# Performance work log

Hardware: AMD Instinct MI355X
Metric: run time of the kernel (lower is better)

The kernel has to match this reference:

```python
import jax, jax.numpy as jnp
import numpy as np

B, NQ, L, E, K = 64, 1024, 128, 8192, 2
LN_EPS = 1e-5


def setup_inputs() -> dict:
    key = jax.random.key(0)
    ks = jax.random.split(key, 16)
    s1 = 1.0 / np.sqrt(2 * L + 1)
    s2 = 1.0 / np.sqrt(L)
    s3 = 1.0 / np.sqrt(2 * L)
    return {
        "z0": jax.random.normal(ks[0], (B, L), jnp.float32),
        "edge_index": jax.random.randint(ks[1], (2, E), 0, NQ, jnp.int64),
        "edge_attr": jax.random.normal(ks[2], (E,), jnp.float32),
        "n_qubits": NQ,
        # edge MLP params, stacked over K message-passing rounds
        "e_w1": jax.random.normal(ks[3], (K, L, 2 * L + 1), jnp.float32) * s1,
        "e_b1": jnp.zeros((K, L), jnp.float32),
        "e_w2": jax.random.normal(ks[4], (K, L, L), jnp.float32) * s2,
        "e_b2": jnp.zeros((K, L), jnp.float32),
        # node MLP params
        "n_w1": jax.random.normal(ks[5], (K, L, 2 * L), jnp.float32) * s3,
        "n_b1": jnp.zeros((K, L), jnp.float32),
        "ln_g": jnp.ones((K, L), jnp.float32),
        "ln_b": jnp.zeros((K, L), jnp.float32),
        "n_w2": jax.random.normal(ks[6], (K, L, L), jnp.float32) * s2,
        "n_b2": jnp.zeros((K, L), jnp.float32),
    }


def reference(z0, edge_index, edge_attr, n_qubits,
              e_w1, e_b1, e_w2, e_b2,
              n_w1, n_b1, ln_g, ln_b, n_w2, n_b2):
    b, l = z0.shape
    src, tgt = edge_index[0], edge_index[1]
    e_ = src.shape[0]
    # broadcast latent z0 to every node: h [B, N, L]
    h = jnp.broadcast_to(z0[:, None, :], (b, n_qubits, l))
    e = jnp.broadcast_to(edge_attr[None, :, None], (b, e_, 1))  # [B, E, 1]
    k_rounds = e_w1.shape[0]
    for k in range(k_rounds):
        hi = h[:, src, :]  # gather source node feats [B, E, L]
        hj = h[:, tgt, :]  # gather target node feats [B, E, L]
        inp_e = jnp.concatenate([hi, hj, e], axis=-1)  # [B, E, 2L+1]
        m = jax.nn.relu(inp_e @ e_w1[k].T + e_b1[k]) @ e_w2[k].T + e_b2[k]
        # scatter_add messages back to source nodes
        m_agg = jnp.zeros_like(h).at[:, src, :].add(m)
        inp_n = jnp.concatenate([h, m_agg], axis=-1)  # [B, N, 2L]
        x = jax.nn.relu(inp_n @ n_w1[k].T + n_b1[k])
        mu = x.mean(axis=-1, keepdims=True)
        var = ((x - mu) ** 2).mean(axis=-1, keepdims=True)
        x = (x - mu) * jax.lax.rsqrt(var + LN_EPS) * ln_g[k] + ln_b[k]
        # Dropout(p=0.1) is identity in eval mode
        h = x @ n_w2[k].T + n_b2[k] + h  # residual
    return h.mean(axis=1)  # [B, L]
```

## Files before the change

### kernel.cpp

```cpp
#include <hip/hip_runtime.h>

#define B_   64
#define NQ_  1024
#define L_   128
#define E_   8192
#define M_   (B_*NQ_)
#define LDP  136

typedef unsigned short u16;
typedef unsigned int   u32;
typedef __attribute__((ext_vector_type(8))) short short8;
typedef __attribute__((ext_vector_type(4))) float floatx4;

#define WVB() __builtin_amdgcn_wave_barrier()

__device__ __forceinline__ u16 f2bf(float f) {
    union { float f; u32 u; } v; v.f = f;
    return (u16)((v.u + 0x7fffu + ((v.u >> 16) & 1u)) >> 16);
}
__device__ __forceinline__ float bf2f(u16 u) {
    union { u32 u; float f; } v; v.u = ((u32)u) << 16;
    return v.f;
}
__device__ __forceinline__ floatx4 mfma16(short8 a, short8 b, floatx4 c) {
    return __builtin_amdgcn_mfma_f32_16x16x32_bf16(a, b, c, 0, 0, 0);
}
__device__ __forceinline__ short8 gfrag(const u16* base, int r0, int kb, int lane) {
    return *(const short8*)(base + (size_t)(r0 + (lane & 15)) * 128 + kb * 32 + (lane >> 4) * 8);
}
__device__ __forceinline__ short8 sfrag(const u16* t, int r0, int kb, int lane) {
    return *(const short8*)(t + (r0 + (lane & 15)) * LDP + kb * 32 + (lane >> 4) * 8);
}
__device__ __forceinline__ short8 frag_cvt(const float* base, int r0, int ld, int kb, int lane) {
    const float* p = base + (size_t)(r0 + (lane & 15)) * ld + kb * 32 + (lane >> 4) * 8;
    short8 s;
#pragma unroll
    for (int j = 0; j < 8; ++j) s[j] = (short)f2bf(p[j]);
    return s;
}
__device__ __forceinline__ void tile_store(u16* t, const floatx4* acc, int lane) {
    int col = lane & 15, qd = lane >> 4;
#pragma unroll
    for (int nt = 0; nt < 8; ++nt)
#pragma unroll
        for (int r = 0; r < 4; ++r)
            t[(qd * 4 + r) * LDP + nt * 16 + col] = f2bf(acc[nt][r]);
}
__device__ __forceinline__ void tile_flush(const u16* t, u16* g, int lane) {
#pragma unroll
    for (int it = 0; it < 4; ++it) {
        int chunk = it * 64 + lane, row = chunk >> 4, c8 = chunk & 15;
        *(uint4*)(g + (size_t)row * 128 + c8 * 8) = *(const uint4*)(t + row * LDP + c8 * 8);
    }
}
__device__ __forceinline__ void stage_w(u16* wbuf, const u16* g, int tid) {
    const uint4* g4 = (const uint4*)g;
#pragma unroll
    for (int i = 0; i < 8; ++i) {
        int idx = tid + i * 256, row = idx >> 4, c8 = idx & 15;
        *(uint4*)&wbuf[row * LDP + c8 * 8] = g4[idx];
    }
}

__global__ __launch_bounds__(256) void k_setup(const int* __restrict__ ei,
                                               const float* __restrict__ attr,
                                               const float* __restrict__ z0,
                                               const float* __restrict__ e_w1,
                                               const float* __restrict__ e_b1,
                                               const float* __restrict__ e_w2,
                                               const float* __restrict__ e_b2,
                                               const float* __restrict__ n_w1,
                                               const float* __restrict__ n_b1,
                                               const float* __restrict__ n_w2,
                                               const float* __restrict__ n_b2,
                                               int* __restrict__ ofs,
                                               int* __restrict__ tgt_s,
                                               float* __restrict__ a_s,
                                               float* __restrict__ degf,
                                               u16* __restrict__ wb,
                                               float* __restrict__ wl,
                                               float* __restrict__ vb2,
                                               float* __restrict__ rx,
                                               float* __restrict__ rci,
                                               float* __restrict__ rcj,
                                               u16* __restrict__ ci0,
                                               u16* __restrict__ cj0) {
    __shared__ __align__(16) char smem[52608];
    int tid = threadIdx.x, blk = blockIdx.x;
    int lane = tid & 63, w = tid >> 6, col = lane & 15, qd = lane >> 4;

    if (blk == 0) {
        int* cnt  = (int*)smem;
        int* wsum = cnt + 1024;
        int* flag = wsum + 8;
#pragma unroll
        for (int i = 0; i < 4; ++i) cnt[tid + i * 256] = 0;
        if (tid == 0) *flag = 1;
        __syncthreads();
        if (tid < 100 && ei[2 * tid + 1] != 0) atomicAnd(flag, 0);
        __syncthreads();
        int i64 = *flag;
        for (int e = tid; e < E_; e += 256) {
            int s = i64 ? ei[2 * e] : ei[e];
            atomicAdd(&cnt[s], 1);
        }
        __syncthreads();
        int q0 = tid * 4;
        int c0 = cnt[q0], c1 = cnt[q0 + 1], c2 = cnt[q0 + 2], c3 = cnt[q0 + 3];
        int tsum = c0 + c1 + c2 + c3, incl = tsum;
#pragma unroll
        for (int o = 1; o < 64; o <<= 1) {
            int t = __shfl_up(incl, o, 64);
            if (lane >= o) incl += t;
        }
        if (lane == 63) wsum[w] = incl;
        __syncthreads();
        int wo = 0;
        for (int i = 0; i < w; ++i) wo += wsum[i];
        int base = wo + incl - tsum;
        ofs[q0] = base; ofs[q0 + 1] = base + c0;
        ofs[q0 + 2] = base + c0 + c1; ofs[q0 + 3] = base + c0 + c1 + c2;
        degf[q0] = (float)c0; degf[q0 + 1] = (float)c1;
        degf[q0 + 2] = (float)c2; degf[q0 + 3] = (float)c3;
        if (tid == 0) ofs[NQ_] = E_;
        __syncthreads();
        cnt[q0] = base; cnt[q0 + 1] = base + c0;
        cnt[q0 + 2] = base + c0 + c1; cnt[q0 + 3] = base + c0 + c1 + c2;
        __syncthreads();
        for (int e = tid; e < E_; e += 256) {
            int s = i64 ? ei[2 * e]        : ei[e];
            int t = i64 ? ei[2 * (E_ + e)] : ei[E_ + e];
            int p = atomicAdd(&cnt[s], 1);
            tgt_s[p] = t;
            a_s[p]   = attr[e];
        }
    } else if (blk <= 3) {
        const float* src; int ld, off; u16* dst;
        if (blk == 1)      { src = n_w2;         ld = 128; off = 0; dst = wb + 1 * 16384; }
        else if (blk == 2) { src = n_w2 + 16384; ld = 128; off = 0; dst = wb + 6 * 16384; }
        else               { src = n_w1 + 32768; ld = 256; off = 0; dst = wb + 4 * 16384; }
        for (int idx = tid; idx < 16384; idx += 256) {
            int n = idx >> 7, kk = idx & 127;
            dst[idx] = f2bf(src[n * ld + off + kk]);
        }
    } else if (blk <= 7) {
        const float* P; const float* Q; int ldp; u16* D;
        if (blk == 4)      { P = n_w1 + 128;           ldp = 256; Q = e_w2;         D = wb;              }
        else if (blk == 5) { P = n_w1 + 32768 + 128;   ldp = 256; Q = e_w2 + 16384; D = wb + 5 * 16384;  }
        else if (blk == 6) { P = e_w1 + 128 * 257;     ldp = 257; Q = n_w2;         D = wb + 2 * 16384;  }
        else               { P = e_w1 + 128 * 257 + 128; ldp = 257; Q = n_w2;       D = wb + 3 * 16384;  }
        u16* qt = (u16*)smem;
        u16* tl = (u16*)(smem + 34816);
        for (int idx = tid; idx < 16384; idx += 256) {
            int c = idx >> 7, kd = idx & 127;
            qt[kd * LDP + c] = f2bf(Q[idx]);
        }
        __syncthreads();
        for (int t = 0; t < 2; ++t) {
            int r0 = (w * 2 + t) * 16;
            floatx4 acc[8] = {};
#pragma unroll
            for (int kb = 0; kb < 4; ++kb) {
                short8 a = frag_cvt(P, r0, ldp, kb, lane);
#pragma unroll
                for (int nt = 0; nt < 8; ++nt)
                    acc[nt] = mfma16(a, sfrag(qt, nt * 16, kb, lane), acc[nt]);
            }
            u16* slot = tl + w * 16 * LDP;
            tile_store(slot, acc, lane); WVB();
            tile_flush(slot, D + (size_t)r0 * 128, lane); WVB();
        }
    } else if (blk == 8) {
        int r0 = w * 16;
        floatx4 acc[8] = {};
#pragma unroll
        for (int kb = 0; kb < 4; ++kb) {
            short8 a = frag_cvt(z0, r0, 128, kb, lane);
#pragma unroll
            for (int nt = 0; nt < 8; ++nt)
                acc[nt] = mfma16(a, frag_cvt(n_w1, nt * 16, 256, kb, lane), acc[nt]);
        }
#pragma unroll
        for (int nt = 0; nt < 8; ++nt) {
            int cg = nt * 16 + col; float bv = n_b1[cg];
#pragma unroll
            for (int r = 0; r < 4; ++r) rx[(r0 + qd * 4 + r) * 128 + cg] = acc[nt][r] + bv;
        }
    } else if (blk == 9 || blk == 10) {
        int r0 = w * 16;
        const float* Wp = (blk == 9) ? (e_w1 + 128 * 257) : (e_w1 + 128 * 257 + 128);
        float* dst = (blk == 9) ? rci : rcj;
        floatx4 acc[8] = {};
#pragma unroll
        for (int kb = 0; kb < 4; ++kb) {
            short8 a;
            int rr = (r0 + (lane & 15)) * 128, kk = kb * 32 + (lane >> 4) * 8;
#pragma unroll
            for (int j = 0; j < 8; ++j) a[j] = (short)f2bf(z0[rr + kk + j] + n_b2[kk + j]);
#pragma unroll
            for (int nt = 0; nt < 8; ++nt)
                acc[nt] = mfma16(a, frag_cvt(Wp, nt * 16, 257, kb, lane), acc[nt]);
        }
#pragma unroll
        for (int nt = 0; nt < 8; ++nt) {
            int cg = nt * 16 + col;
            float bv = (blk == 9) ? e_b1[128 + cg] : 0.0f;
#pragma unroll
            for (int r = 0; r < 4; ++r) dst[(r0 + qd * 4 + r) * 128 + cg] = acc[nt][r] + bv;
        }
    } else if (blk == 11) {
        u16* tl = (u16*)(smem + 34816);
        int r0 = w * 16;
        floatx4 a1[8] = {}, a2[8] = {};
#pragma unroll
        for (int kb = 0; kb < 4; ++kb) {
            short8 a = frag_cvt(z0, r0, 128, kb, lane);
#pragma unroll
            for (int nt = 0; nt < 8; ++nt) {
                a1[nt] = mfma16(a, frag_cvt(e_w1,       nt * 16, 257, kb, lane), a1[nt]);
                a2[nt] = mfma16(a, frag_cvt(e_w1 + 128, nt * 16, 257, kb, lane), a2[nt]);
            }
        }
#pragma unroll
        for (int nt = 0; nt < 8; ++nt) {
            float bv = e_b1[nt * 16 + col];
#pragma unroll
            for (int r = 0; r < 4; ++r) a1[nt][r] += bv;
        }
        u16* slot = tl + w * 16 * LDP;
        tile_store(slot, a1, lane); WVB();
        tile_flush(slot, ci0 + (size_t)r0 * 128, lane); WVB();
        tile_store(slot, a2, lane); WVB();
        tile_flush(slot, cj0 + (size_t)r0 * 128, lane);
    } else {
        int k = tid >> 7, c = tid & 127;
        float s = 0.0f;
        for (int n = 0; n < 128; ++n)
            s += n_w1[k * 32768 + c * 256 + 128 + n] * e_b2[k * 128 + n];
        vb2[tid] = s;
        wl[tid]  = e_w1[k * 128 * 257 + c * 257 + 256];
    }
}

__global__ __launch_bounds__(256) void k_edge(const u16* __restrict__ ci,
                                              const u16* __restrict__ cj,
                                              int ci_bs, int ci_qs,
                                              int cj_bs, int cj_ts,
                                              const int* __restrict__ ofs,
                                              const int* __restrict__ tgt_s,
                                              const float* __restrict__ a_s,
                                              const float* __restrict__ wl,
                                              u16* __restrict__ S) {
    int tid = threadIdx.x, lane = tid & 63, w = tid >> 6;
    int gw = blockIdx.x * 4 + w;
    int q = gw & (NQ_ - 1), b0 = (gw >> 10) * 4;
    const u32* cjp0 = (const u32*)cj + (size_t)(b0 + 0) * cj_bs;
    const u32* cjp1 = (const u32*)cj + (size_t)(b0 + 1) * cj_bs;
    const u32* cjp2 = (const u32*)cj + (size_t)(b0 + 2) * cj_bs;
    const u32* cjp3 = (const u32*)cj + (size_t)(b0 + 3) * cj_bs;
    float cix[4], ciy[4];
#pragma unroll
    for (int i = 0; i < 4; ++i) {
        u32 cv = ((const u32*)ci)[(size_t)(b0 + i) * ci_bs + (size_t)q * ci_qs + lane];
        cix[i] = bf2f((u16)(cv & 0xffff)); ciy[i] = bf2f((u16)(cv >> 16));
    }
    float2 wl2 = ((const float2*)wl)[lane];
    int st = ofs[q], en = ofs[q + 1];
    float ax[4] = {0, 0, 0, 0}, ay[4] = {0, 0, 0, 0};
    for (int idx = st; idx < en; ++idx) {
        int t = tgt_s[idx];
        float a = a_s[idx];
        size_t ro = (size_t)t * cj_ts + lane;
        u32 j0 = cjp0[ro], j1 = cjp1[ro], j2 = cjp2[ro], j3 = cjp3[ro];
        float wx = a * wl2.x, wy = a * wl2.y;
        ax[0] += fmaxf(cix[0] + bf2f((u16)(j0 & 0xffff)) + wx, 0.f);
        ay[0] += fmaxf(ciy[0] + bf2f((u16)(j0 >> 16))    + wy, 0.f);
        ax[1] += fmaxf(cix[1] + bf2f((u16)(j1 & 0xffff)) + wx, 0.f);
        ay[1] += fmaxf(ciy[1] + bf2f((u16)(j1 >> 16))    + wy, 0.f);
        ax[2] += fmaxf(cix[2] + bf2f((u16)(j2 & 0xffff)) + wx, 0.f);
        ay[2] += fmaxf(ciy[2] + bf2f((u16)(j2 >> 16))    + wy, 0.f);
        ax[3] += fmaxf(cix[3] + bf2f((u16)(j3 & 0xffff)) + wx, 0.f);
        ay[3] += fmaxf(ciy[3] + bf2f((u16)(j3 >> 16))    + wy, 0.f);
    }
    u32* Sp = (u32*)S;
#pragma unroll
    for (int i = 0; i < 4; ++i)
        Sp[((size_t)(b0 + i) * NQ_ + q) * 64 + lane] =
            (u32)f2bf(ax[i]) | ((u32)f2bf(ay[i]) << 16);
}

__global__ __launch_bounds__(256, 2) void k_node0(const u16* __restrict__ S,
                                                  const u16* __restrict__ wb,
                                                  const float* __restrict__ rx,
                                                  const float* __restrict__ vb2,
                                                  const float* __restrict__ degf,
                                                  const float* __restrict__ z0,
                                                  const float* __restrict__ n_b2,
                                                  const float* __restrict__ rci,
                                                  const float* __restrict__ rcj,
                                                  const float* __restrict__ g,
                                                  const float* __restrict__ bb,
                                                  u16* __restrict__ hbf,
                                                  u16* __restrict__ ci1,
                                                  u16* __restrict__ cj1,
                                                  float* __restrict__ out) {
    __shared__ u16 wbuf[128 * LDP];
    __shared__ u16 xt[8][16 * LDP];
    __shared__ float rsum[4][128];
    int tid = threadIdx.x, lane = tid & 63, w = tid >> 6;
    int col = lane & 15, qd = lane >> 4;
    int rowbase = blockIdx.x * 128 + w * 32;
    int b = blockIdx.x >> 3;

    stage_w(wbuf, wb, tid);
    __syncthreads();
    floatx4 xa[2][8] = {};
#pragma unroll
    for (int kb = 0; kb < 4; ++kb) {
        short8 Bv[8];
#pragma unroll
        for (int nt = 0; nt < 8; ++nt) Bv[nt] = sfrag(wbuf, nt * 16, kb, lane);
#pragma unroll
        for (int t = 0; t < 2; ++t) {
            short8 a = gfrag(S, rowbase + t * 16, kb, lane);
#pragma unroll
            for (int nt = 0; nt < 8; ++nt) xa[t][nt] = mfma16(a, Bv[nt], xa[t][nt]);
        }
    }
#pragma unroll
    for (int t = 0; t < 2; ++t) {
#pragma unroll
        for (int nt = 0; nt < 8; ++nt) {
            int cg = nt * 16 + col;
            float base = rx[b * 128 + cg], vb = vb2[cg];
#pragma unroll
            for (int r = 0; r < 4; ++r) {
                int row = rowbase + t * 16 + qd * 4 + r;
                xa[t][nt][r] = fmaxf(xa[t][nt][r] + base + degf[row & (NQ_ - 1)] * vb, 0.f);
            }
        }
#pragma unroll
        for (int r = 0; r < 4; ++r) {
            float s = 0.f, s2 = 0.f;
#pragma unroll
            for (int nt = 0; nt < 8; ++nt) { float v = xa[t][nt][r]; s += v; s2 += v * v; }
#pragma unroll
            for (int o = 1; o < 16; o <<= 1) { s += __shfl_xor(s, o, 64); s2 += __shfl_xor(s2, o, 64); }
            float mu = s * (1.f / 128.f), var = s2 * (1.f / 128.f) - mu * mu;
            float rs = rsqrtf(var + 1e-5f);
#pragma unroll
            for (int nt = 0; nt < 8; ++nt) {
                int cg = nt * 16 + col;
                xa[t][nt][r] = (xa[t][nt][r] - mu) * rs * g[cg] + bb[cg];
            }
        }
        tile_store(&xt[w * 2 + t][0], xa[t], lane);
    }
    __syncthreads();

    stage_w(wbuf, wb + 1 * 16384, tid);
    __syncthreads();
    floatx4 ha[2][8] = {};
#pragma unroll
    for (int kb = 0; kb < 4; ++kb) {
        short8 Bv[8];
#pragma unroll
        for (int nt = 0; nt < 8; ++nt) Bv[nt] = sfrag(wbuf, nt * 16, kb, lane);
#pragma unroll
        for (int t = 0; t < 2; ++t) {
            short8 a = sfrag(&xt[w * 2 + t][0], 0, kb, lane);
#pragma unroll
            for (int nt = 0; nt < 8; ++nt) ha[t][nt] = mfma16(a, Bv[nt], ha[t][nt]);
        }
    }
    float s8[8] = {0, 0, 0, 0, 0, 0, 0, 0};
#pragma unroll
    for (int t = 0; t < 2; ++t)
#pragma unroll
        for (int nt = 0; nt < 8; ++nt) {
            int cg = nt * 16 + col;
            float hp = z0[b * 128 + cg] + n_b2[cg];
#pragma unroll
            for (int r = 0; r < 4; ++r) {
                float hv = ha[t][nt][r] + hp;
                ha[t][nt][r] = hv;
                s8[nt] += hv;
            }
        }
#pragma unroll
    for (int nt = 0; nt < 8; ++nt) {
        s8[nt] += __shfl_xor(s8[nt], 16, 64);
        s8[nt] += __shfl_xor(s8[nt], 32, 64);
    }
    if (lane < 16) {
#pragma unroll
        for (int nt = 0; nt < 8; ++nt) rsum[w][nt * 16 + lane] = s8[nt];
    }
    __syncthreads();
    if (tid < 128) {
        float v = rsum[0][tid] + rsum[1][tid] + rsum[2][tid] + rsum[3][tid];
        atomicAdd(out + b * 128 + tid, v * (1.f / 1024.f));
    }
#pragma unroll
    for (int t = 0; t < 2; ++t) tile_store(wbuf + (w * 2 + t) * 16 * LDP, ha[t], lane);
    WVB();
#pragma unroll
    for (int t = 0; t < 2; ++t)
        tile_flush(wbuf + (w * 2 + t) * 16 * LDP, hbf + (size_t)(rowbase + t * 16) * 128, lane);
    __syncthreads();

    stage_w(wbuf, wb + 2 * 16384, tid);
    __syncthreads();
    floatx4 ca[2][8] = {};
#pragma unroll
    for (int kb = 0; kb < 4; ++kb) {
        short8 Bv[8];
#pragma unroll
        for (int nt = 0; nt < 8; ++nt) Bv[nt] = sfrag(wbuf, nt * 16, kb, lane);
#pragma unroll
        for (int t = 0; t < 2; ++t) {
            short8 a = sfrag(&xt[w * 2 + t][0], 0, kb, lane);
#pragma unroll
            for (int nt = 0; nt < 8; ++nt) ca[t][nt] = mfma16(a, Bv[nt], ca[t][nt]);
        }
    }
#pragma unroll
    for (int t = 0; t < 2; ++t)
#pragma unroll
        for (int nt = 0; nt < 8; ++nt) {
            float rc = rci[b * 128 + nt * 16 + col];
#pragma unroll
            for (int r = 0; r < 4; ++r) ca[t][nt][r] += rc;
        }
    __syncthreads();
#pragma unroll
    for (int t = 0; t < 2; ++t) tile_store(wbuf + (w * 2 + t) * 16 * LDP, ca[t], lane);
    WVB();
#pragma unroll
    for (int t = 0; t < 2; ++t)
        tile_flush(wbuf + (w * 2 + t) * 16 * LDP, ci1 + (size_t)(rowbase + t * 16) * 128, lane);
    __syncthreads();

    stage_w(wbuf, wb + 3 * 16384, tid);
    __syncthreads();
    floatx4 da[2][8] = {};
#pragma unroll
    for (int kb = 0; kb < 4; ++kb) {
        short8 Bv[8];
#pragma unroll
        for (int nt = 0; nt < 8; ++nt) Bv[nt] = sfrag(wbuf, nt * 16, kb, lane);
#pragma unroll
        for (int t = 0; t < 2; ++t) {
            short8 a = sfrag(&xt[w * 2 + t][0], 0, kb, lane);
#pragma unroll
            for (int nt = 0; nt < 8; ++nt) da[t][nt] = mfma16(a, Bv[nt], da[t][nt]);
        }
    }
#pragma unroll
    for (int t = 0; t < 2; ++t)
#pragma unroll
        for (int nt = 0; nt < 8; ++nt) {
            float rc = rcj[b * 128 + nt * 16 + col];
#pragma unroll
            for (int r = 0; r < 4; ++r) da[t][nt][r] += rc;
        }
    __syncthreads();
#pragma unroll
    for (int t = 0; t < 2; ++t) tile_store(wbuf + (w * 2 + t) * 16 * LDP, da[t], lane);
    WVB();
#pragma unroll
    for (int t = 0; t < 2; ++t)
        tile_flush(wbuf + (w * 2 + t) * 16 * LDP, cj1 + (size_t)(rowbase + t * 16) * 128, lane);
}

__global__ __launch_bounds__(256, 2) void k_node1(const u16* __restrict__ S,
                                                  const u16* __restrict__ hbf,
                                                  const u16* __restrict__ wb,
                                                  const float* __restrict__ vb2,
                                                  const float* __restrict__ degf,
                                                  const float* __restrict__ n_b1,
                                                  const float* __restrict__ g,
                                                  const float* __restrict__ bb,
                                                  const float* __restrict__ n_b2,
                                                  float* __restrict__ out) {
    __shared__ u16 wbuf[128 * LDP];
    __shared__ u16 xt[8][16 * LDP];
    __shared__ float rsum[4][128];
    int tid = threadIdx.x, lane = tid & 63, w = tid >> 6;
    int col = lane & 15, qd = lane >> 4;
    int rowbase = blockIdx.x * 128 + w * 32;
    int b = blockIdx.x >> 3;

    stage_w(wbuf, wb + 4 * 16384, tid);
    __syncthreads();
    floatx4 xa[2][8] = {};
#pragma unroll
    for (int kb = 0; kb < 4; ++kb) {
        short8 Bv[8];
#pragma unroll
        for (int nt = 0; nt < 8; ++nt) Bv[nt] = sfrag(wbuf, nt * 16, kb, lane);
#pragma unroll
        for (int t = 0; t < 2; ++t) {
            short8 a = gfrag(hbf, rowbase + t * 16, kb, lane);
#pragma unroll
            for (int nt = 0; nt < 8; ++nt) xa[t][nt] = mfma16(a, Bv[nt], xa[t][nt]);
        }
    }
    __syncthreads();
    stage_w(wbuf, wb + 5 * 16384, tid);
    __syncthreads();
#pragma unroll
    for (int kb = 0; kb < 4; ++kb) {
        short8 Bv[8];
#pragma unroll
        for (int nt = 0; nt < 8; ++nt) Bv[nt] = sfrag(wbuf, nt * 16, kb, lane);
#pragma unroll
        for (int t = 0; t < 2; ++t) {
            short8 a = gfrag(S, rowbase + t * 16, kb, lane);
#pragma unroll
            for (int nt = 0; nt < 8; ++nt) xa[t][nt] = mfma16(a, Bv[nt], xa[t][nt]);
        }
    }
#pragma unroll
    for (int t = 0; t < 2; ++t) {
#pragma unroll
        for (int nt = 0; nt < 8; ++nt) {
            int cg = nt * 16 + col;
            float base = n_b1[cg], vb = vb2[cg];
#pragma unroll
            for (int r = 0; r < 4; ++r) {
                int row = rowbase + t * 16 + qd * 4 + r;
                xa[t][nt][r] = fmaxf(xa[t][nt][r] + base + degf[row & (NQ_ - 1)] * vb, 0.f);
            }
        }
#pragma unroll
        for (int r = 0; r < 4; ++r) {
            float s = 0.f, s2 = 0.f;
#pragma unroll
            for (int nt = 0; nt < 8; ++nt) { float v = xa[t][nt][r]; s += v; s2 += v * v; }
#pragma unroll
            for (int o = 1; o < 16; o <<= 1) { s += __shfl_xor(s, o, 64); s2 += __shfl_xor(s2, o, 64); }
            float mu = s * (1.f / 128.f), var = s2 * (1.f / 128.f) - mu * mu;
            float rs = rsqrtf(var + 1e-5f);
#pragma unroll
            for (int nt = 0; nt < 8; ++nt) {
                int cg = nt * 16 + col;
                xa[t][nt][r] = (xa[t][nt][r] - mu) * rs * g[cg] + bb[cg];
            }
        }
        tile_store(&xt[w * 2 + t][0], xa[t], lane);
    }
    __syncthreads();

    stage_w(wbuf, wb + 6 * 16384, tid);
    __syncthreads();
    floatx4 ma[2][8] = {};
#pragma unroll
    for (int kb = 0; kb < 4; ++kb) {
        short8 Bv[8];
#pragma unroll
        for (int nt = 0; nt < 8; ++nt) Bv[nt] = sfrag(wbuf, nt * 16, kb, lane);
#pragma unroll
        for (int t = 0; t < 2; ++t) {
            short8 a = sfrag(&xt[w * 2 + t][0], 0, kb, lane);
#pragma unroll
            for (int nt = 0; nt < 8; ++nt) ma[t][nt] = mfma16(a, Bv[nt], ma[t][nt]);
        }
    }
    float s8[8] = {0, 0, 0, 0, 0, 0, 0, 0};
#pragma unroll
    for (int t = 0; t < 2; ++t)
#pragma unroll
        for (int nt = 0; nt < 8; ++nt)
#pragma unroll
            for (int r = 0; r < 4; ++r) s8[nt] += ma[t][nt][r];
#pragma unroll
    for (int nt = 0; nt < 8; ++nt) {
        s8[nt] += __shfl_xor(s8[nt], 16, 64);
        s8[nt] += __shfl_xor(s8[nt], 32, 64);
    }
    if (lane < 16) {
#pragma unroll
        for (int nt = 0; nt < 8; ++nt) rsum[w][nt * 16 + lane] = s8[nt];
    }
    __syncthreads();
    if (tid < 128) {
        float v = rsum[0][tid] + rsum[1][tid] + rsum[2][tid] + rsum[3][tid];
        atomicAdd(out + b * 128 + tid, v * (1.f / 1024.f) + n_b2[tid] * 0.125f);
    }
}

extern "C" void kernel_launch(void* const* d_in, const int* in_sizes, int n_in,
                              void* d_out, int out_size, void* d_ws, size_t ws_size,
                              hipStream_t stream) {
    const float* z0    = (const float*)d_in[0];
    const int*   ei    = (const int*)d_in[1];
    const float* attr  = (const float*)d_in[2];
    const float* e_w1  = (const float*)d_in[4];
    const float* e_b1  = (const float*)d_in[5];
    const float* e_w2  = (const float*)d_in[6];
    const float* e_b2  = (const float*)d_in[7];
    const float* n_w1  = (const float*)d_in[8];
    const float* n_b1  = (const float*)d_in[9];
    const float* ln_g  = (const float*)d_in[10];
    const float* ln_b  = (const float*)d_in[11];
    const float* n_w2  = (const float*)d_in[12];
    const float* n_b2  = (const float*)d_in[13];
    float* out = (float*)d_out;

    const size_t H = (size_t)M_ * L_;
    float* f    = (float*)d_ws;
    float* degf = f;
    float* a_s  = degf + 1024;
    float* wl   = a_s + 8192;
    float* vb2  = wl + 256;
    float* rx   = vb2 + 256;
    float* rci  = rx + 8192;
    float* rcj  = rci + 8192;
    int*   ofs   = (int*)(rcj + 8192);
    int*   tgt_s = ofs + 1056;
    u16*   wb    = (u16*)(tgt_s + 8192);
    u16*   ci0   = wb + 7 * 16384;
    u16*   cj0   = ci0 + 8192;
    u16*   S     = cj0 + 8192;
    u16*   hbf   = S + H;
    u16*   ci1   = hbf + H;
    u16*   cj1   = ci1 + H;

    hipMemsetAsync(out, 0, 8192 * sizeof(float), stream);

    k_setup<<<13, 256, 0, stream>>>(ei, attr, z0, e_w1, e_b1, e_w2, e_b2,
                                    n_w1, n_b1, n_w2, n_b2,
                                    ofs, tgt_s, a_s, degf, wb, wl, vb2,
                                    rx, rci, rcj, ci0, cj0);

    k_edge<<<4096, 256, 0, stream>>>(ci0, cj0, 64, 0, 64, 0,
                                     ofs, tgt_s, a_s, wl, S);
    k_node0<<<512, 256, 0, stream>>>(S, wb, rx, vb2, degf, z0, n_b2,
                                     rci, rcj, ln_g, ln_b,
                                     hbf, ci1, cj1, out);
    k_edge<<<4096, 256, 0, stream>>>(ci1, cj1, NQ_ * 64, 64, NQ_ * 64, 64,
                                     ofs, tgt_s, a_s, wl + 128, S);
    k_node1<<<512, 256, 0, stream>>>(S, hbf, wb, vb2 + 128, degf,
                                     n_b1 + 128, ln_g + 128, ln_b + 128,
                                     n_b2 + 128, out);
}
```

Before: 197.1 us.

## Fold round-0 node output into next-round projections and specialize first edge pass

Round 0's node output is no longer materialized as h. k_node0 projects the layer-normed activations directly through the folded round-1 weights (h-part of n_w1, ci, cj) and accumulates their per-batch mean into mx0. The final mean is then reconstructed algebraically from mx0 through n_w2 in k_node1. The first edge pass uses a template specialization that exploits the constant per-batch node features, so it skips the target gather by merging the ci and cj contributions into one tensor. Each edge warp now handles 8 batches instead of 4, halving the grid. This moves work between stages, and using an extra bf16 intermediate risks small precision changes.

Result: faster. 190.9 us (-3.2%).

```diff
diff --git a/kernel.cpp b/kernel.cpp
--- a/kernel.cpp
+++ b/kernel.cpp
@@ -83,8 +83,9 @@
                                                float* __restrict__ rx,
                                                float* __restrict__ rci,
                                                float* __restrict__ rcj,
-                                               u16* __restrict__ ci0,
-                                               u16* __restrict__ cj0) {
+                                               float* __restrict__ rh,
+                                               float* __restrict__ mx0,
+                                               u16* __restrict__ c0t) {
     __shared__ __align__(16) char smem[52608];
     int tid = threadIdx.x, blk = blockIdx.x;
     int lane = tid & 63, w = tid >> 6, col = lane & 15, qd = lane >> 4;
@@ -130,25 +131,23 @@
         for (int e = tid; e < E_; e += 256) {
             int s = i64 ? ei[2 * e]        : ei[e];
             int t = i64 ? ei[2 * (E_ + e)] : ei[E_ + e];
-            int p = atomicAdd(&cnt[s], 1);
-            tgt_s[p] = t;
-            a_s[p]   = attr[e];
-        }
-    } else if (blk <= 3) {
-        const float* src; int ld, off; u16* dst;
-        if (blk == 1)      { src = n_w2;         ld = 128; off = 0; dst = wb + 1 * 16384; }
-        else if (blk == 2) { src = n_w2 + 16384; ld = 128; off = 0; dst = wb + 6 * 16384; }
-        else               { src = n_w1 + 32768; ld = 256; off = 0; dst = wb + 4 * 16384; }
-        for (int idx = tid; idx < 16384; idx += 256) {
-            int n = idx >> 7, kk = idx & 127;
-            dst[idx] = f2bf(src[n * ld + off + kk]);
-        }
+            int pos = atomicAdd(&cnt[s], 1);
+            tgt_s[pos] = t;
+            a_s[pos]   = attr[e];
+        }
+    } else if (blk <= 2) {
+        const float* src = (blk == 1) ? n_w2 : (n_w2 + 16384);
+        u16* dst = wb + ((blk == 1) ? 1 : 6) * 16384;
+        for (int idx = tid; idx < 16384; idx += 256) dst[idx] = f2bf(src[idx]);
     } else if (blk <= 7) {
         const float* P; const float* Q; int ldp; u16* D;
-        if (blk == 4)      { P = n_w1 + 128;           ldp = 256; Q = e_w2;         D = wb;              }
-        else if (blk == 5) { P = n_w1 + 32768 + 128;   ldp = 256; Q = e_w2 + 16384; D = wb + 5 * 16384;  }
-        else if (blk == 6) { P = e_w1 + 128 * 257;     ldp = 257; Q = n_w2;         D = wb + 2 * 16384;  }
-        else               { P = e_w1 + 128 * 257 + 128; ldp = 257; Q = n_w2;       D = wb + 3 * 16384;  }
+        switch (blk) {
+            case 3: P = n_w1 + 128;             ldp = 256; Q = e_w2;         D = wb;             break;
+            case 4: P = n_w1 + 32768 + 128;     ldp = 256; Q = e_w2 + 16384; D = wb + 5 * 16384; break;
+            case 5: P = e_w1 + 128 * 257;       ldp = 257; Q = n_w2;         D = wb + 2 * 16384; break;
+            case 6: P = e_w1 + 128 * 257 + 128; ldp = 257; Q = n_w2;         D = wb + 3 * 16384; break;
+            default:P = n_w1 + 32768;           ldp = 256; Q = n_w2;         D = wb + 4 * 16384; break;
+        }
         u16* qt = (u16*)smem;
         u16* tl = (u16*)(smem + 34816);
         for (int idx = tid; idx < 16384; idx += 256) {
@@ -186,10 +185,12 @@
 #pragma unroll
             for (int r = 0; r < 4; ++r) rx[(r0 + qd * 4 + r) * 128 + cg] = acc[nt][r] + bv;
         }
-    } else if (blk == 9 || blk == 10) {
+    } else if (blk <= 11) {
         int r0 = w * 16;
-        const float* Wp = (blk == 9) ? (e_w1 + 128 * 257) : (e_w1 + 128 * 257 + 128);
-        float* dst = (blk == 9) ? rci : rcj;
+        const float* Wp; int ld; const float* bias; float* dst;
+        if (blk == 9)       { Wp = e_w1 + 128 * 257;       ld = 257; bias = e_b1 + 128; dst = rci; }
+        else if (blk == 10) { Wp = e_w1 + 128 * 257 + 128; ld = 257; bias = nullptr;    dst = rcj; }
+        else                { Wp = n_w1 + 32768;           ld = 256; bias = n_b1 + 128; dst = rh;  }
         floatx4 acc[8] = {};
 #pragma unroll
         for (int kb = 0; kb < 4; ++kb) {
@@ -199,26 +200,26 @@
             for (int j = 0; j < 8; ++j) a[j] = (short)f2bf(z0[rr + kk + j] + n_b2[kk + j]);
 #pragma unroll
             for (int nt = 0; nt < 8; ++nt)
-                acc[nt] = mfma16(a, frag_cvt(Wp, nt * 16, 257, kb, lane), acc[nt]);
+                acc[nt] = mfma16(a, frag_cvt(Wp, nt * 16, ld, kb, lane), acc[nt]);
         }
 #pragma unroll
         for (int nt = 0; nt < 8; ++nt) {
             int cg = nt * 16 + col;
-            float bv = (blk == 9) ? e_b1[128 + cg] : 0.0f;
+            float bv = bias ? bias[cg] : 0.0f;
 #pragma unroll
             for (int r = 0; r < 4; ++r) dst[(r0 + qd * 4 + r) * 128 + cg] = acc[nt][r] + bv;
         }
-    } else if (blk == 11) {
+    } else if (blk == 12) {
         u16* tl = (u16*)(smem + 34816);
         int r0 = w * 16;
-        floatx4 a1[8] = {}, a2[8] = {};
+        floatx4 a1[8] = {};
 #pragma unroll
         for (int kb = 0; kb < 4; ++kb) {
             short8 a = frag_cvt(z0, r0, 128, kb, lane);
 #pragma unroll
             for (int nt = 0; nt < 8; ++nt) {
                 a1[nt] = mfma16(a, frag_cvt(e_w1,       nt * 16, 257, kb, lane), a1[nt]);
-                a2[nt] = mfma16(a, frag_cvt(e_w1 + 128, nt * 16, 257, kb, lane), a2[nt]);
+                a1[nt] = mfma16(a, frag_cvt(e_w1 + 128, nt * 16, 257, kb, lane), a1[nt]);
             }
         }
 #pragma unroll
@@ -229,9 +230,7 @@
         }
         u16* slot = tl + w * 16 * LDP;
         tile_store(slot, a1, lane); WVB();
-        tile_flush(slot, ci0 + (size_t)r0 * 128, lane); WVB();
-        tile_store(slot, a2, lane); WVB();
-        tile_flush(slot, cj0 + (size_t)r0 * 128, lane);
+        tile_flush(slot, c0t + (size_t)r0 * 128, lane);
     } else {
         int k = tid >> 7, c = tid & 127;
         float s = 0.0f;
@@ -239,13 +238,13 @@
             s += n_w1[k * 32768 + c * 256 + 128 + n] * e_b2[k * 128 + n];
         vb2[tid] = s;
         wl[tid]  = e_w1[k * 128 * 257 + c * 257 + 256];
-    }
-}
-
+        for (int i = tid; i < 8192; i += 256) mx0[i] = 0.0f;
+    }
+}
+
+template <bool R0>
 __global__ __launch_bounds__(256) void k_edge(const u16* __restrict__ ci,
                                               const u16* __restrict__ cj,
-                                              int ci_bs, int ci_qs,
-                                              int cj_bs, int cj_ts,
                                               const int* __restrict__ ofs,
                                               const int* __restrict__ tgt_s,
                                               const float* __restrict__ a_s,
@@ -253,39 +252,55 @@
                                               u16* __restrict__ S) {
     int tid = threadIdx.x, lane = tid & 63, w = tid >> 6;
     int gw = blockIdx.x * 4 + w;
-    int q = gw & (NQ_ - 1), b0 = (gw >> 10) * 4;
-    const u32* cjp0 = (const u32*)cj + (size_t)(b0 + 0) * cj_bs;
-    const u32* cjp1 = (const u32*)cj + (size_t)(b0 + 1) * cj_bs;
-    const u32* cjp2 = (const u32*)cj + (size_t)(b0 + 2) * cj_bs;
-    const u32* cjp3 = (const u32*)cj + (size_t)(b0 + 3) * cj_bs;
-    float cix[4], ciy[4];
-#pragma unroll
-    for (int i = 0; i < 4; ++i) {
-        u32 cv = ((const u32*)ci)[(size_t)(b0 + i) * ci_bs + (size_t)q * ci_qs + lane];
-        cix[i] = bf2f((u16)(cv & 0xffff)); ciy[i] = bf2f((u16)(cv >> 16));
-    }
+    int q = gw & (NQ_ - 1), bg = gw >> 10;
+    int bl[8];
+#pragma unroll
+    for (int i = 0; i < 4; ++i) { bl[i] = bg * 4 + i; bl[i + 4] = bg * 4 + i + 32; }
     float2 wl2 = ((const float2*)wl)[lane];
     int st = ofs[q], en = ofs[q + 1];
-    float ax[4] = {0, 0, 0, 0}, ay[4] = {0, 0, 0, 0};
-    for (int idx = st; idx < en; ++idx) {
-        int t = tgt_s[idx];
-        float a = a_s[idx];
-        size_t ro = (size_t)t * cj_ts + lane;
-        u32 j0 = cjp0[ro], j1 = cjp1[ro], j2 = cjp2[ro], j3 = cjp3[ro];
-        float wx = a * wl2.x, wy = a * wl2.y;
-        ax[0] += fmaxf(cix[0] + bf2f((u16)(j0 & 0xffff)) + wx, 0.f);
-        ay[0] += fmaxf(ciy[0] + bf2f((u16)(j0 >> 16))    + wy, 0.f);
-        ax[1] += fmaxf(cix[1] + bf2f((u16)(j1 & 0xffff)) + wx, 0.f);
-        ay[1] += fmaxf(ciy[1] + bf2f((u16)(j1 >> 16))    + wy, 0.f);
-        ax[2] += fmaxf(cix[2] + bf2f((u16)(j2 & 0xffff)) + wx, 0.f);
-        ay[2] += fmaxf(ciy[2] + bf2f((u16)(j2 >> 16))    + wy, 0.f);
-        ax[3] += fmaxf(cix[3] + bf2f((u16)(j3 & 0xffff)) + wx, 0.f);
-        ay[3] += fmaxf(ciy[3] + bf2f((u16)(j3 >> 16))    + wy, 0.f);
+    float ax[8] = {}, ay[8] = {};
+    if (R0) {
+        float cx[8], cy[8];
+#pragma unroll
+        for (int i = 0; i < 8; ++i) {
+            u32 cv = ((const u32*)ci)[(size_t)bl[i] * 64 + lane];
+            cx[i] = bf2f((u16)(cv & 0xffff)); cy[i] = bf2f((u16)(cv >> 16));
+        }
+        for (int idx = st; idx < en; ++idx) {
+            float a = a_s[idx];
+            float wx = a * wl2.x, wy = a * wl2.y;
+#pragma unroll
+            for (int i = 0; i < 8; ++i) {
+                ax[i] += fmaxf(cx[i] + wx, 0.f);
+                ay[i] += fmaxf(cy[i] + wy, 0.f);
+            }
+        }
+    } else {
+        const u32* cjp[8];
+        float cx[8], cy[8];
+#pragma unroll
+        for (int i = 0; i < 8; ++i) {
+            cjp[i] = (const u32*)cj + (size_t)bl[i] * NQ_ * 64;
+            u32 cv = ((const u32*)ci)[((size_t)bl[i] * NQ_ + q) * 64 + lane];
+            cx[i] = bf2f((u16)(cv & 0xffff)); cy[i] = bf2f((u16)(cv >> 16));
+        }
+        for (int idx = st; idx < en; ++idx) {
+            int t = tgt_s[idx];
+            float a = a_s[idx];
+            size_t ro = (size_t)t * 64 + lane;
+            float wx = a * wl2.x, wy = a * wl2.y;
+#pragma unroll
+            for (int i = 0; i < 8; ++i) {
+                u32 jv = cjp[i][ro];
+                ax[i] += fmaxf(cx[i] + bf2f((u16)(jv & 0xffff)) + wx, 0.f);
+                ay[i] += fmaxf(cy[i] + bf2f((u16)(jv >> 16))    + wy, 0.f);
+            }
+        }
     }
     u32* Sp = (u32*)S;
 #pragma unroll
-    for (int i = 0; i < 4; ++i)
-        Sp[((size_t)(b0 + i) * NQ_ + q) * 64 + lane] =
+    for (int i = 0; i < 8; ++i)
+        Sp[((size_t)bl[i] * NQ_ + q) * 64 + lane] =
             (u32)f2bf(ax[i]) | ((u32)f2bf(ay[i]) << 16);
 }
 
@@ -294,15 +309,134 @@
                                                   const float* __restrict__ rx,
                                                   const float* __restrict__ vb2,
                                                   const float* __restrict__ degf,
+                                                  const float* __restrict__ rci,
+                                                  const float* __restrict__ rcj,
+                                                  const float* __restrict__ rh,
+                                                  const float* __restrict__ g,
+                                                  const float* __restrict__ bb,
+                                                  float* __restrict__ mx0,
+                                                  u16* __restrict__ t1,
+                                                  u16* __restrict__ ci1,
+                                                  u16* __restrict__ cj1) {
+    __shared__ u16 wbuf[128 * LDP];
+    __shared__ u16 xt[8][16 * LDP];
+    __shared__ float rsum[4][128];
+    int tid = threadIdx.x, lane = tid & 63, w = tid >> 6;
+    int col = lane & 15, qd = lane >> 4;
+    int rowbase = blockIdx.x * 128 + w * 32;
+    int b = blockIdx.x >> 3;
+
+    stage_w(wbuf, wb, tid);
+    __syncthreads();
+    floatx4 xa[2][8] = {};
+#pragma unroll
+    for (int kb = 0; kb < 4; ++kb) {
+        short8 Bv[8];
+#pragma unroll
+        for (int nt = 0; nt < 8; ++nt) Bv[nt] = sfrag(wbuf, nt * 16, kb, lane);
+#pragma unroll
+        for (int t = 0; t < 2; ++t) {
+            short8 a = gfrag(S, rowbase + t * 16, kb, lane);
+#pragma unroll
+            for (int nt = 0; nt < 8; ++nt) xa[t][nt] = mfma16(a, Bv[nt], xa[t][nt]);
+        }
+    }
+    float s8[8] = {};
+#pragma unroll
+    for (int t = 0; t < 2; ++t) {
+#pragma unroll
+        for (int nt = 0; nt < 8; ++nt) {
+            int cg = nt * 16 + col;
+            float base = rx[b * 128 + cg], vb = vb2[cg];
+#pragma unroll
+            for (int r = 0; r < 4; ++r) {
+                int row = rowbase + t * 16 + qd * 4 + r;
+                xa[t][nt][r] = fmaxf(xa[t][nt][r] + base + degf[row & (NQ_ - 1)] * vb, 0.f);
+            }
+        }
+#pragma unroll
+        for (int r = 0; r < 4; ++r) {
+            float s = 0.f, s2 = 0.f;
+#pragma unroll
+            for (int nt = 0; nt < 8; ++nt) { float v = xa[t][nt][r]; s += v; s2 += v * v; }
+#pragma unroll
+            for (int o = 1; o < 16; o <<= 1) { s += __shfl_xor(s, o, 64); s2 += __shfl_xor(s2, o, 64); }
+            float mu = s * (1.f / 128.f), var = s2 * (1.f / 128.f) - mu * mu;
+            float rs = rsqrtf(var + 1e-5f);
+#pragma unroll
+            for (int nt = 0; nt < 8; ++nt) {
+                int cg = nt * 16 + col;
+                float xv = (xa[t][nt][r] - mu) * rs * g[cg] + bb[cg];
+                xa[t][nt][r] = xv;
+                s8[nt] += xv;
+            }
+        }
+        tile_store(&xt[w * 2 + t][0], xa[t], lane);
+    }
+#pragma unroll
+    for (int nt = 0; nt < 8; ++nt) {
+        s8[nt] += __shfl_xor(s8[nt], 16, 64);
+        s8[nt] += __shfl_xor(s8[nt], 32, 64);
+    }
+    if (lane < 16) {
+#pragma unroll
+        for (int nt = 0; nt < 8; ++nt) rsum[w][nt * 16 + lane] = s8[nt];
+    }
+    __syncthreads();
+    if (tid < 128) {
+        float v = rsum[0][tid] + rsum[1][tid] + rsum[2][tid] + rsum[3][tid];
+        atomicAdd(mx0 + b * 128 + tid, v);
+    }
+
+#pragma unroll
+    for (int ph = 0; ph < 3; ++ph) {
+        const u16* Wsl = wb + ((ph == 0) ? 4 : (ph == 1) ? 2 : 3) * 16384;
+        const float* rt = (ph == 0) ? rh : (ph == 1) ? rci : rcj;
+        u16* dstg = (ph == 0) ? t1 : (ph == 1) ? ci1 : cj1;
+        __syncthreads();
+        stage_w(wbuf, Wsl, tid);
+        __syncthreads();
+        floatx4 ca[2][8] = {};
+#pragma unroll
+        for (int kb = 0; kb < 4; ++kb) {
+            short8 Bv[8];
+#pragma unroll
+            for (int nt = 0; nt < 8; ++nt) Bv[nt] = sfrag(wbuf, nt * 16, kb, lane);
+#pragma unroll
+            for (int t = 0; t < 2; ++t) {
+                short8 a = sfrag(&xt[w * 2 + t][0], 0, kb, lane);
+#pragma unroll
+                for (int nt = 0; nt < 8; ++nt) ca[t][nt] = mfma16(a, Bv[nt], ca[t][nt]);
+            }
+        }
+#pragma unroll
+        for (int t = 0; t < 2; ++t)
+#pragma unroll
+            for (int nt = 0; nt < 8; ++nt) {
+                float rc = rt[b * 128 + nt * 16 + col];
+#pragma unroll
+                for (int r = 0; r < 4; ++r) ca[t][nt][r] += rc;
+            }
+        __syncthreads();
+#pragma unroll
+        for (int t = 0; t < 2; ++t) tile_store(wbuf + (w * 2 + t) * 16 * LDP, ca[t], lane);
+        WVB();
+#pragma unroll
+        for (int t = 0; t < 2; ++t)
+            tile_flush(wbuf + (w * 2 + t) * 16 * LDP, dstg + (size_t)(rowbase + t * 16) * 128, lane);
+    }
+}
+
+__global__ __launch_bounds__(256, 2) void k_node1(const u16* __restrict__ S,
+                                                  const u16* __restrict__ t1,
+                                                  const u16* __restrict__ wb,
+                                                  const float* __restrict__ vb2,
+                                                  const float* __restrict__ degf,
+                                                  const float* __restrict__ g,
+                                                  const float* __restrict__ bb,
                                                   const float* __restrict__ z0,
                                                   const float* __restrict__ n_b2,
-                                                  const float* __restrict__ rci,
-                                                  const float* __restrict__ rcj,
-                                                  const float* __restrict__ g,
-                                                  const float* __restrict__ bb,
-                                                  u16* __restrict__ hbf,
-                                                  u16* __restrict__ ci1,
-                                                  u16* __restrict__ cj1,
+                                                  const float* __restrict__ mx0,
                                                   float* __restrict__ out) {
     __shared__ u16 wbuf[128 * LDP];
     __shared__ u16 xt[8][16 * LDP];
@@ -312,7 +446,7 @@
     int rowbase = blockIdx.x * 128 + w * 32;
     int b = blockIdx.x >> 3;
 
-    stage_w(wbuf, wb, tid);
+    stage_w(wbuf, wb + 5 * 16384, tid);
     __syncthreads();
     floatx4 xa[2][8] = {};
 #pragma unroll
@@ -332,11 +466,12 @@
 #pragma unroll
         for (int nt = 0; nt < 8; ++nt) {
             int cg = nt * 16 + col;
-            float base = rx[b * 128 + cg], vb = vb2[cg];
+            float vb = vb2[cg];
 #pragma unroll
             for (int r = 0; r < 4; ++r) {
                 int row = rowbase + t * 16 + qd * 4 + r;
-                xa[t][nt][r] = fmaxf(xa[t][nt][r] + base + degf[row & (NQ_ - 1)] * vb, 0.f);
+                float tv = bf2f(t1[(size_t)row * 128 + cg]);
+                xa[t][nt][r] = fmaxf(xa[t][nt][r] + tv + degf[row & (NQ_ - 1)] * vb, 0.f);
             }
         }
 #pragma unroll
@@ -358,9 +493,9 @@
     }
     __syncthreads();
 
-    stage_w(wbuf, wb + 1 * 16384, tid);
+    stage_w(wbuf, wb + 6 * 16384, tid);
     __syncthreads();
-    floatx4 ha[2][8] = {};
+    floatx4 ma[2][8] = {};
 #pragma unroll
     for (int kb = 0; kb < 4; ++kb) {
         short8 Bv[8];
@@ -370,23 +505,16 @@
         for (int t = 0; t < 2; ++t) {
             short8 a = sfrag(&xt[w * 2 + t][0], 0, kb, lane);
 #pragma unroll
-            for (int nt = 0; nt < 8; ++nt) ha[t][nt] = mfma16(a, Bv[nt], ha[t][nt]);
-        }
-    }
-    float s8[8] = {0, 0, 0, 0, 0, 0, 0, 0};
+            for (int nt = 0; nt < 8; ++nt) ma[t][nt] = mfma16(a, Bv[nt], ma[t][nt]);
+        }
+    }
+    float s8[8] = {};
 #pragma unroll
     for (int t = 0; t < 2; ++t)
 #pragma unroll
-        for (int nt = 0; nt < 8; ++nt) {
-            int cg = nt * 16 + col;
-            float hp = z0[b * 128 + cg] + n_b2[cg];
-#pragma unroll
-            for (int r = 0; r < 4; ++r) {
-                float hv = ha[t][nt][r] + hp;
-                ha[t][nt][r] = hv;
-                s8[nt] += hv;
-            }
-        }
+        for (int nt = 0; nt < 8; ++nt)
+#pragma unroll
+            for (int r = 0; r < 4; ++r) s8[nt] += ma[t][nt][r];
 #pragma unroll
     for (int nt = 0; nt < 8; ++nt) {
         s8[nt] += __shfl_xor(s8[nt], 16, 64);
@@ -401,247 +529,71 @@
         float v = rsum[0][tid] + rsum[1][tid] + rsum[2][tid] + rsum[3][tid];
         atomicAdd(out + b * 128 + tid, v * (1.f / 1024.f));
     }
-#pragma unroll
-    for (int t = 0; t < 2; ++t) tile_store(wbuf + (w * 2 + t) * 16 * LDP, ha[t], lane);
-    WVB();
-#pragma unroll
-    for (int t = 0; t < 2; ++t)
-        tile_flush(wbuf + (w * 2 + t) * 16 * LDP, hbf + (size_t)(rowbase + t * 16) * 128, lane);
-    __syncthreads();
-
-    stage_w(wbuf, wb + 2 * 16384, tid);
-    __syncthreads();
-    floatx4 ca[2][8] = {};
-#pragma unroll
-    for (int kb = 0; kb < 4; ++kb) {
-        short8 Bv[8];
-#pragma unroll
-        for (int nt = 0; nt < 8; ++nt) Bv[nt] = sfrag(wbuf, nt * 16, kb, lane);
-#pragma unroll
-        for (int t = 0; t < 2; ++t) {
-            short8 a = sfrag(&xt[w * 2 + t][0], 0, kb, lane);
-#pragma unroll
-            for (int nt = 0; nt < 8; ++nt) ca[t][nt] = mfma16(a, Bv[nt], ca[t][nt]);
-        }
-    }
-#pragma unroll
-    for (int t = 0; t < 2; ++t)
-#pragma unroll
-        for (int nt = 0; nt < 8; ++nt) {
-            float rc = rci[b * 128 + nt * 16 + col];
-#pragma unroll
-            for (int r = 0; r < 4; ++r) ca[t][nt][r] += rc;
-        }
-    __syncthreads();
-#pragma unroll
-    for (int t = 0; t < 2; ++t) tile_store(wbuf + (w * 2 + t) * 16 * LDP, ca[t], lane);
-    WVB();
-#pragma unroll
-    for (int t = 0; t < 2; ++t)
-        tile_flush(wbuf + (w * 2 + t) * 16 * LDP, ci1 + (size_t)(rowbase + t * 16) * 128, lane);
-    __syncthreads();
-
-    stage_w(wbuf, wb + 3 * 16384, tid);
-    __syncthreads();
-    floatx4 da[2][8] = {};
-#pragma unroll
-    for (int kb = 0; kb < 4; ++kb) {
-        short8 Bv[8];
-#pragma unroll
-        for (int nt = 0; nt < 8; ++nt) Bv[nt] = sfrag(wbuf, nt * 16, kb, lane);
-#pragma unroll
-        for (int t = 0; t < 2; ++t) {
-            short8 a = sfrag(&xt[w * 2 + t][0], 0, kb, lane);
-#pragma unroll
-            for (int nt = 0; nt < 8; ++nt) da[t][nt] = mfma16(a, Bv[nt], da[t][nt]);
-        }
-    }
-#pragma unroll
-    for (int t = 0; t < 2; ++t)
-#pragma unroll
-        for (int nt = 0; nt < 8; ++nt) {
-            float rc = rcj[b * 128 + nt * 16 + col];
-#pragma unroll
-            for (int r = 0; r < 4; ++r) da[t][nt][r] += rc;
-        }
-    __syncthreads();
-#pragma unroll
-    for (int t = 0; t < 2; ++t) tile_store(wbuf + (w * 2 + t) * 16 * LDP, da[t], lane);
-    WVB();
-#pragma unroll
-    for (int t = 0; t < 2; ++t)
-        tile_flush(wbuf + (w * 2 + t) * 16 * LDP, cj1 + (size_t)(rowbase + t * 16) * 128, lane);
-}
-
-__global__ __launch_bounds__(256, 2) void k_node1(const u16* __restrict__ S,
-                                                  const u16* __restrict__ hbf,
-                                                  const u16* __restrict__ wb,
-                                                  const float* __restrict__ vb2,
-                                                  const float* __restrict__ degf,
-                                                  const float* __restrict__ n_b1,
-                                                  const float* __restrict__ g,
-                                                  const float* __restrict__ bb,
-                                                  const float* __restrict__ n_b2,
-                                                  float* __restrict__ out) {
-    __shared__ u16 wbuf[128 * LDP];
-    __shared__ u16 xt[8][16 * LDP];
-    __shared__ float rsum[4][128];
-    int tid = threadIdx.x, lane = tid & 63, w = tid >> 6;
-    int col = lane & 15, qd = lane >> 4;
-    int rowbase = blockIdx.x * 128 + w * 32;
-    int b = blockIdx.x >> 3;
-
-    stage_w(wbuf, wb + 4 * 16384, tid);
-    __syncthreads();
-    floatx4 xa[2][8] = {};
-#pragma unroll
-    for (int kb = 0; kb < 4; ++kb) {
-        short8 Bv[8];
-#pragma unroll
-        for (int nt = 0; nt < 8; ++nt) Bv[nt] = sfrag(wbuf, nt * 16, kb, lane);
-#pragma unroll
-        for (int t = 0; t < 2; ++t) {
-            short8 a = gfrag(hbf, rowbase + t * 16, kb, lane);
-#pragma unroll
-            for (int nt = 0; nt < 8; ++nt) xa[t][nt] = mfma16(a, Bv[nt], xa[t][nt]);
-        }
-    }
-    __syncthreads();
-    stage_w(wbuf, wb + 5 * 16384, tid);
-    __syncthreads();
-#pragma unroll
-    for (int kb = 0; kb < 4; ++kb) {
-        short8 Bv[8];
-#pragma unroll
-        for (int nt = 0; nt < 8; ++nt) Bv[nt] = sfrag(wbuf, nt * 16, kb, lane);
-#pragma unroll
-        for (int t = 0; t < 2; ++t) {
-            short8 a = gfrag(S, rowbase + t * 16, kb, lane);
-#pragma unroll
-            for (int nt = 0; nt < 8; ++nt) xa[t][nt] = mfma16(a, Bv[nt], xa[t][nt]);
-        }
-    }
-#pragma unroll
-    for (int t = 0; t < 2; ++t) {
-#pragma unroll
-        for (int nt = 0; nt < 8; ++nt) {
-            int cg = nt * 16 + col;
-            float base = n_b1[cg], vb = vb2[cg];
-#pragma unroll
-            for (int r = 0; r < 4; ++r) {
-                int row = rowbase + t * 16 + qd * 4 + r;
-                xa[t][nt][r] = fmaxf(xa[t][nt][r] + base + degf[row & (NQ_ - 1)] * vb, 0.f);
-            }
-        }
-#pragma unroll
-        for (int r = 0; r < 4; ++r) {
-            float s = 0.f, s2 = 0.f;
-#pragma unroll
-            for (int nt = 0; nt < 8; ++nt) { float v = xa[t][nt][r]; s += v; s2 += v * v; }
-#pragma unroll
-            for (int o = 1; o < 16; o <<= 1) { s += __shfl_xor(s, o, 64); s2 += __shfl_xor(s2, o, 64); }
-            float mu = s * (1.f / 128.f), var = s2 * (1.f / 128.f) - mu * mu;
-            float rs = rsqrtf(var + 1e-5f);
-#pragma unroll
-            for (int nt = 0; nt < 8; ++nt) {
-                int cg = nt * 16 + col;
-                xa[t][nt][r] = (xa[t][nt][r] - mu) * rs * g[cg] + bb[cg];
-            }
-        }
-        tile_store(&xt[w * 2 + t][0], xa[t], lane);
-    }
-    __syncthreads();
-
-    stage_w(wbuf, wb + 6 * 16384, tid);
-    __syncthreads();
-    floatx4 ma[2][8] = {};
-#pragma unroll
-    for (int kb = 0; kb < 4; ++kb) {
-        short8 Bv[8];
-#pragma unroll
-        for (int nt = 0; nt < 8; ++nt) Bv[nt] = sfrag(wbuf, nt * 16, kb, lane);
-#pragma unroll
-        for (int t = 0; t < 2; ++t) {
-            short8 a = sfrag(&xt[w * 2 + t][0], 0, kb, lane);
-#pragma unroll
-            for (int nt = 0; nt < 8; ++nt) ma[t][nt] = mfma16(a, Bv[nt], ma[t][nt]);
-        }
-    }
-    float s8[8] = {0, 0, 0, 0, 0, 0, 0, 0};
-#pragma unroll
-    for (int t = 0; t < 2; ++t)
-#pragma unroll
-        for (int nt = 0; nt < 8; ++nt)
-#pragma unroll
-            for (int r = 0; r < 4; ++r) s8[nt] += ma[t][nt][r];
-#pragma unroll
-    for (int nt = 0; nt < 8; ++nt) {
-        s8[nt] += __shfl_xor(s8[nt], 16, 64);
-        s8[nt] += __shfl_xor(s8[nt], 32, 64);
-    }
-    if (lane < 16) {
-#pragma unroll
-        for (int nt = 0; nt < 8; ++nt) rsum[w][nt * 16 + lane] = s8[nt];
-    }
-    __syncthreads();
-    if (tid < 128) {
-        float v = rsum[0][tid] + rsum[1][tid] + rsum[2][tid] + rsum[3][tid];
-        atomicAdd(out + b * 128 + tid, v * (1.f / 1024.f) + n_b2[tid] * 0.125f);
+
+    if ((blockIdx.x & 7) == 0 && tid < 128) {
+        int c = tid;
+        const u16* w2s = wb + 1 * 16384;
+        const float* mx = mx0 + b * 128;
+        float s = 0.f;
+#pragma unroll 4
+        for (int k = 0; k < 128; ++k) s += mx[k] * bf2f(w2s[c * 128 + k]);
+        float acc = z0[b * 128 + c] + n_b2[c] + n_b2[128 + c] + s * (1.f / 1024.f);
+        atomicAdd(out + b * 128 + c, acc);
     }
 }
 
 extern "C" void kernel_launch(void* const* d_in, const int* in_sizes, int n_in,
                               void* d_out, int out_size, void* d_ws, size_t ws_size,
                               hipStream_t stream) {
-    const float* z0    = (const float*)d_in[0];
-    const int*   ei    = (const int*)d_in[1];
-    const float* attr  = (const float*)d_in[2];
-    const float* e_w1  = (const float*)d_in[4];
-    const float* e_b1  = (const float*)d_in[5];
-    const float* e_w2  = (const float*)d_in[6];
-    const float* e_b2  = (const float*)d_in[7];
-    const float* n_w1  = (const float*)d_in[8];
-    const float* n_b1  = (const float*)d_in[9];
-    const float* ln_g  = (const float*)d_in[10];
-    const float* ln_b  = (const float*)d_in[11];
-    const float* n_w2  = (const float*)d_in[12];
-    const float* n_b2  = (const float*)d_in[13];
+    const float* z0   = (const float*)d_in[0];
+    const int*   ei   = (const int*)d_in[1];
+    const float* attr = (const float*)d_in[2];
+    const float* e_w1 = (const float*)d_in[4];
+    const float* e_b1 = (const float*)d_in[5];
+    const float* e_w2 = (const float*)d_in[6];
+    const float* e_b2 = (const float*)d_in[7];
+    const float* n_w1 = (const float*)d_in[8];
+    const float* n_b1 = (const float*)d_in[9];
+    const float* ln_g = (const float*)d_in[10];
+    const float* ln_b = (const float*)d_in[11];
+    const float* n_w2 = (const float*)d_in[12];
+    const float* n_b2 = (const float*)d_in[13];
     float* out = (float*)d_out;
 
     const size_t H = (size_t)M_ * L_;
-    float* f    = (float*)d_ws;
-    float* degf = f;
-    float* a_s  = degf + 1024;
-    float* wl   = a_s + 8192;
-    float* vb2  = wl + 256;
-    float* rx   = vb2 + 256;
-    float* rci  = rx + 8192;
-    float* rcj  = rci + 8192;
-    int*   ofs   = (int*)(rcj + 8192);
+    float* f     = (float*)d_ws;
+    float* degf  = f;
+    float* a_s   = f + 1024;
+    float* wl    = a_s + 8192;
+    float* vb2   = wl + 256;
+    float* rx    = vb2 + 256;
+    float* rci   = rx + 8192;
+    float* rcj   = rci + 8192;
+    float* rh    = rcj + 8192;
+    float* mx0   = rh + 8192;
+    int*   ofs   = (int*)(mx0 + 8192);
     int*   tgt_s = ofs + 1056;
     u16*   wb    = (u16*)(tgt_s + 8192);
-    u16*   ci0   = wb + 7 * 16384;
-    u16*   cj0   = ci0 + 8192;
-    u16*   S     = cj0 + 8192;
-    u16*   hbf   = S + H;
-    u16*   ci1   = hbf + H;
+    u16*   c0t   = wb + 7 * 16384;
+    u16*   S     = c0t + 8192;
+    u16*   t1    = S + H;
+    u16*   ci1   = t1 + H;
     u16*   cj1   = ci1 + H;
 
     hipMemsetAsync(out, 0, 8192 * sizeof(float), stream);
 
-    k_setup<<<13, 256, 0, stream>>>(ei, attr, z0, e_w1, e_b1, e_w2, e_b2,
+    k_setup<<<14, 256, 0, stream>>>(ei, attr, z0, e_w1, e_b1, e_w2, e_b2,
                                     n_w1, n_b1, n_w2, n_b2,
                                     ofs, tgt_s, a_s, degf, wb, wl, vb2,
-                                    rx, rci, rcj, ci0, cj0);
-
-    k_edge<<<4096, 256, 0, stream>>>(ci0, cj0, 64, 0, 64, 0,
-                                     ofs, tgt_s, a_s, wl, S);
-    k_node0<<<512, 256, 0, stream>>>(S, wb, rx, vb2, degf, z0, n_b2,
-                                     rci, rcj, ln_g, ln_b,
-                                     hbf, ci1, cj1, out);
-    k_edge<<<4096, 256, 0, stream>>>(ci1, cj1, NQ_ * 64, 64, NQ_ * 64, 64,
-                                     ofs, tgt_s, a_s, wl + 128, S);
-    k_node1<<<512, 256, 0, stream>>>(S, hbf, wb, vb2 + 128, degf,
-                                     n_b1 + 128, ln_g + 128, ln_b + 128,
-                                     n_b2 + 128, out);
-}
+                                    rx, rci, rcj, rh, mx0, c0t);
+
+    k_edge<true><<<2048, 256, 0, stream>>>(c0t, nullptr, ofs, tgt_s, a_s, wl, S);
+
+    k_node0<<<512, 256, 0, stream>>>(S, wb, rx, vb2, degf, rci, rcj, rh,
+                                     ln_g, ln_b, mx0, t1, ci1, cj1);
+
+    k_edge<false><<<2048, 256, 0, stream>>>(ci1, cj1, ofs, tgt_s, a_s, wl + 128, S);
+
+    k_node1<<<512, 256, 0, stream>>>(S, t1, wb, vb2 + 128, degf,
+                                     ln_g + 128, ln_b + 128, z0, n_b2, mx0, out);
+}
```
